# Optimization experiments

Hardware: AMD Instinct MI355X
Metric: run time of the kernel (lower is better)

The kernel has to match this reference:

```python
import jax, jax.numpy as jnp
import numpy as np

B, N, X, Y, W1, W2, D = 2, 6, 8, 8, 8, 8, 128
H, DH = 4, 32
L = X * Y          # number of windows
QT = N * W1 * W2   # tokens per window
EPS = 1e-5


def _ln(x, g, b):
    m = x.mean(-1, keepdims=True)
    v = ((x - m) ** 2).mean(-1, keepdims=True)
    return (x - m) * jax.lax.rsqrt(v + EPS) * g + b


def _win(t):
    # b n x y w1 w2 d -> b (x y) (n w1 w2) d
    return t.transpose(0, 2, 3, 1, 4, 5, 6).reshape(B, L, QT, D)


def setup_inputs() -> dict:
    key = jax.random.key(0)
    ks = jax.random.split(key, 12)
    s = 0.02
    inp = {
        'q': jax.random.normal(ks[0], (B, N, X, Y, W1, W2, D), jnp.float32),
        'k': jax.random.normal(ks[1], (B, N, X, Y, W1, W2, D), jnp.float32),
        'v': jax.random.normal(ks[2], (B, N, X, Y, W1, W2, D), jnp.float32),
        'skip': jax.random.normal(ks[3], (B, X, Y, W1, W2, D), jnp.float32),
        'gq': jnp.ones((D,), jnp.float32), 'betq': jnp.zeros((D,), jnp.float32),
        'gk': jnp.ones((D,), jnp.float32), 'betk': jnp.zeros((D,), jnp.float32),
        'gv': jnp.ones((D,), jnp.float32), 'betv': jnp.zeros((D,), jnp.float32),
        'wq': jax.random.normal(ks[4], (D, H * DH), jnp.float32) * s,
        'bq': jnp.zeros((H * DH,), jnp.float32),
        'wk': jax.random.normal(ks[5], (D, H * DH), jnp.float32) * s,
        'bk': jnp.zeros((H * DH,), jnp.float32),
        'wv': jax.random.normal(ks[6], (D, H * DH), jnp.float32) * s,
        'bv': jnp.zeros((H * DH,), jnp.float32),
        'wp': jax.random.normal(ks[7], (H * DH, D), jnp.float32) * s,
        'bp': jnp.zeros((D,), jnp.float32),
    }
    return inp


def reference(q, k, v, skip, gq, betq, gk, betk, gv, betv,
              wq, bq, wk, bk, wv, bv, wp, bp):
    scale = DH ** -0.5
    qw, kw, vw = _win(q), _win(k), _win(v)
    # LayerNorm + Linear QKV, split heads: (b, l, T, h, dh)
    qh = (_ln(qw, gq, betq) @ wq + bq).reshape(B, L, QT, H, DH)
    kh = (_ln(kw, gk, betk) @ wk + bk).reshape(B, L, QT, H, DH)
    vh = (_ln(vw, gv, betv) @ wv + bv).reshape(B, L, QT, H, DH)
    dot = scale * jnp.einsum('blqhd,blkhd->bhlqk', qh, kh)
    att = jax.nn.softmax(dot, axis=-1)
    a = jnp.einsum('bhlqk,blkhd->blqhd', att, vh).reshape(B, L, QT, H * DH)
    # b (x y) (n w1 w2) d -> b n x y w1 w2 d
    a = a.reshape(B, X, Y, N, W1, W2, H * DH).transpose(0, 3, 1, 2, 4, 5, 6)
    z = a @ wp + bp
    z = z.mean(1)  # average over views
    return z + skip
```

## Files before the change

### kernel.cpp

```cpp
#include <hip/hip_runtime.h>


typedef unsigned short u16;
typedef __bf16 bf16x8 __attribute__((ext_vector_type(8)));
typedef __bf16 bf16x4 __attribute__((ext_vector_type(4)));
typedef float  f32x16 __attribute__((ext_vector_type(16)));
typedef unsigned short u16x8 __attribute__((ext_vector_type(8)));
typedef unsigned short u16x4 __attribute__((ext_vector_type(4)));

union U8 { u16x8 u; bf16x8 b; u16x4 h[2]; };

#if __has_builtin(__builtin_amdgcn_exp2f)
#define EXP2(x) __builtin_amdgcn_exp2f(x)
#else
#define EXP2(x) exp2f(x)
#endif

__device__ __forceinline__ f32x16 mfma_bf16(bf16x8 a, bf16x8 b, f32x16 c){
  return __builtin_amdgcn_mfma_f32_32x32x16_bf16(a, b, c, 0, 0, 0);
}


__global__ __launch_bounds__(512) void k_prep(
    const float* __restrict__ wq, const float* __restrict__ bq,
    const float* __restrict__ gq, const float* __restrict__ betq,
    const float* __restrict__ wk, const float* __restrict__ bk,
    const float* __restrict__ gk, const float* __restrict__ betk,
    const float* __restrict__ wv, const float* __restrict__ bv,
    const float* __restrict__ gv, const float* __restrict__ betv,
    const float* __restrict__ wp,
    u16* __restrict__ wqT, u16* __restrict__ wkT, u16* __restrict__ wvT, u16* __restrict__ wpT,
    float* __restrict__ bq2, float* __restrict__ bk2, float* __restrict__ bv2,
    float* __restrict__ uq2, float* __restrict__ uk2, float* __restrict__ uv2)
{
  __shared__ float wls[128*33];
  __shared__ float gls[128], bls[128];
  __shared__ float redb[128], redu[128];
  const float ALPHA_Q = 0.17677669529663687f * 1.4426950408889634f;
  int bid = blockIdx.x, tid = threadIdx.x;
  int wsel = bid >> 2, chunk = bid & 3;
  const float *w, *bb, *g, *bet; u16* wT; float *b2, *u2; float alpha;
  if (wsel == 0){ w=wq; bb=bq; g=gq; bet=betq; wT=wqT; b2=bq2; u2=uq2; alpha=ALPHA_Q; }
  else if (wsel == 1){ w=wk; bb=bk; g=gk; bet=betk; wT=wkT; b2=bk2; u2=uk2; alpha=1.f; }
  else if (wsel == 2){ w=wv; bb=bv; g=gv; bet=betv; wT=wvT; b2=bv2; u2=uv2; alpha=1.f; }
  else { w=wp; bb=nullptr; g=nullptr; bet=nullptr; wT=wpT; b2=nullptr; u2=nullptr; alpha=1.f; }

  if (tid < 128){
    gls[tid] = g ? g[tid] : 1.f;
    bls[tid] = bet ? bet[tid] : 0.f;
  }
  const float4* w4 = (const float4*)w;
  #pragma unroll
  for (int i = 0; i < 2; i++){
    int idx = tid + i*512;
    int row = idx >> 3, f4c = idx & 7;
    float4 x = w4[row*32 + chunk*8 + f4c];
    wls[row*33 + f4c*4 + 0] = x.x;
    wls[row*33 + f4c*4 + 1] = x.y;
    wls[row*33 + f4c*4 + 2] = x.z;
    wls[row*33 + f4c*4 + 3] = x.w;
  }
  __syncthreads();
  if (tid < 128){
    int nl = tid >> 2, qp = tid & 3;
    float sb = 0.f, su = 0.f;
    alignas(16) __bf16 tmp[32];
    #pragma unroll
    for (int kk = 0; kk < 32; kk++){
      int k2 = qp*32 + kk;
      float wv_ = wls[k2*33 + nl];
      float gv_ = gls[k2];
      sb += bls[k2] * wv_;
      su += gv_ * wv_;
      tmp[kk] = (__bf16)(wv_ * gv_ * alpha);
    }
    int n = chunk*32 + nl;
    #pragma unroll
    for (int j = 0; j < 4; j++)
      *(bf16x8*)(wT + n*128 + qp*32 + j*8) = *(bf16x8*)&tmp[j*8];
    redb[tid] = sb; redu[tid] = su;
  }
  __syncthreads();
  if (tid < 128){
    int nl = tid >> 2, qp = tid & 3;
    if (qp == 0 && bb){
      int n = chunk*32 + nl;
      float s = bb[n] + redb[tid] + redb[tid+1] + redb[tid+2] + redb[tid+3];
      float u = redu[tid] + redu[tid+1] + redu[tid+2] + redu[tid+3];
      b2[n] = s * alpha;
      u2[n] = u * alpha;
    }
  }
}

__global__ __launch_bounds__(256) void k_lnproj(
    const float* __restrict__ qg, const float* __restrict__ kg, const float* __restrict__ vg,
    const u16* __restrict__ wqT, const u16* __restrict__ wkT, const u16* __restrict__ wvT,
    const float* __restrict__ bq2, const float* __restrict__ bk2, const float* __restrict__ bv2,
    const float* __restrict__ uq2, const float* __restrict__ uk2, const float* __restrict__ uv2,
    u16* __restrict__ qh, u16* __restrict__ kh, u16* __restrict__ vh)
{
  __shared__ alignas(16) u16 Abf[64*136];
  __shared__ float s1s[64], s2s[64];
  int bid = blockIdx.x, tid = threadIdx.x;
  int which = bid % 3;
  int t = bid / 3;
  int n = t % 6, bl = t / 6;
  const float* src; const u16* wT; const float *b2, *u2; u16* dstb;
  if (which == 0){ src=qg; wT=wqT; b2=bq2; u2=uq2; dstb=qh; }
  else if (which == 1){ src=kg; wT=wkT; b2=bk2; u2=uk2; dstb=kh; }
  else { src=vg; wT=wvT; b2=bv2; u2=uv2; dstb=vh; }
  int b = bl >> 6, l = bl & 63;
  const float4* s4 = (const float4*)(src + (size_t)((b*6 + n)*64 + l)*64*128);
  int row = tid >> 2, j = tid & 3;
  float s1 = 0.f, s2 = 0.f;
  #pragma unroll
  for (int i = 0; i < 8; i++){
    float4 xv = s4[row*32 + i*4 + j];
    s1 += xv.x + xv.y + xv.z + xv.w;
    s2 += xv.x*xv.x + xv.y*xv.y + xv.z*xv.z + xv.w*xv.w;
    bf16x4 pk;
    pk[0] = (__bf16)xv.x; pk[1] = (__bf16)xv.y;
    pk[2] = (__bf16)xv.z; pk[3] = (__bf16)xv.w;
    *(bf16x4*)&Abf[row*136 + (i*4 + j)*4] = pk;
  }
  s1 += __shfl_xor(s1, 1, 64); s1 += __shfl_xor(s1, 2, 64);
  s2 += __shfl_xor(s2, 1, 64); s2 += __shfl_xor(s2, 2, 64);
  if (j == 0){
    float m = s1 * (1.f/128.f);
    float r = rsqrtf(s2 * (1.f/128.f) - m*m + 1e-5f);
    s1s[row] = r;
    s2s[row] = r * m;
  }
  __syncthreads();
  int wave = tid >> 6, lane = tid & 63, lm = lane & 31, lh = lane >> 5;
  bf16x8 bfr[8];
  const u16* wrow = wT + (32*wave + lm)*128 + lh*8;
  #pragma unroll
  for (int ks = 0; ks < 8; ks++) bfr[ks] = *(const bf16x8*)(wrow + ks*16);
  f32x16 acc0, acc1;
  #pragma unroll
  for (int r = 0; r < 16; r++){ acc0[r]=0.f; acc1[r]=0.f; }
  #pragma unroll
  for (int ks = 0; ks < 8; ks++){
    bf16x8 a0 = *(const bf16x8*)&Abf[lm*136       + ks*16 + lh*8];
    bf16x8 a1 = *(const bf16x8*)&Abf[(32+lm)*136  + ks*16 + lh*8];
    acc0 = mfma_bf16(a0, bfr[ks], acc0);
    acc1 = mfma_bf16(a1, bfr[ks], acc1);
  }
  int col = 32*wave + lm;
  float u2c = u2[col], bc = b2[col];
  __syncthreads();
  #pragma unroll
  for (int r = 0; r < 16; r++){
    int row0 = (r&3) + 8*(r>>2) + 4*lh;
    float y0 = s1s[row0]     * acc0[r] - s2s[row0]     * u2c + bc;
    float y1 = s1s[row0+32]  * acc1[r] - s2s[row0+32]  * u2c + bc;
    *(__bf16*)&Abf[row0*136 + col]      = (__bf16)y0;
    *(__bf16*)&Abf[(32+row0)*136 + col] = (__bf16)y1;
  }
  __syncthreads();
  #pragma unroll
  for (int i = 0; i < 4; i++){
    int c = tid + i*256;
    int grp = c >> 8, rw = (c >> 2) & 63, part = c & 3;
    u16x8 val = *(const u16x8*)&Abf[rw*136 + grp*32 + part*8];
    *(u16x8*)(dstb + ((size_t)(bl*4 + grp)*384 + n*64 + rw)*32 + part*8) = val;
  }
}

__global__ __launch_bounds__(768, 3) void k_attn(
    const u16* __restrict__ qh, const u16* __restrict__ kh, const u16* __restrict__ vh,
    u16* __restrict__ abar)
{
  extern __shared__ __align__(16) char smem[];
  int bid = blockIdx.x, tid = threadIdx.x;
  int wave = tid >> 6, lane = tid & 63, lm = lane & 31, lh = lane >> 5;
  int grp = (wave >= 6) ? 1 : 0;
  int n = wave - 6*grp;
  int tl = tid - 384*grp;
  int bh = bid + 256*grp;
  int h = bh & 3, bl = bh >> 2;

  u16*   vts    = (u16*)  (smem + grp*25088);
  float* abar_s = (float*)(smem + 50176 + grp*8192);

  const u16* qb = qh + (size_t)bh * 12288;
  const u16* kb = kh + (size_t)bh * 12288;
  const u16* vb = vh + (size_t)bh * 12288;

  const u16* qbase = qb + (size_t)(n*64 + lm)*32 + lh*8;
  bf16x8 qfA0 = *(const bf16x8*)(qbase);
  bf16x8 qfA1 = *(const bf16x8*)(qbase + 16);
  bf16x8 qfB0 = *(const bf16x8*)(qbase + 32*32);
  bf16x8 qfB1 = *(const bf16x8*)(qbase + 32*32 + 16);

  #pragma unroll
  for (int i = 0; i < 4; i++){
    int c = tl + i*384;
    int key = c >> 2, part = c & 3;
    int u = key & 31, tt = key >> 5;
    int a = u >> 2;
    int anew = (a & 4) | ((a & 1) << 1) | ((a >> 1) & 1);
    int pos = tt*32 + anew*4 + (u & 3);
    u16x8 vv = *(const u16x8*)(vb + key*32 + part*8);
    #pragma unroll
    for (int jj = 0; jj < 8; jj++) vts[(part*8 + jj)*392 + pos] = vv[jj];
  }
  for (int idx = tl; idx < 2048; idx += 384) abar_s[idx] = 0.f;
  __syncthreads();

  const u16* vrow = &vts[lm*392 + 8*lh];
  const u16* krow = kb + lm*32 + lh*8;

  f32x16 oA, oB;
  #pragma unroll
  for (int r = 0; r < 16; r++){ oA[r] = 0.f; oB[r] = 0.f; }
  float sleA = 0.f, sleB = 0.f;

  #pragma unroll
  for (int kt = 0; kt < 12; kt++){
    bf16x8 kf0 = *(const bf16x8*)(krow + kt*1024);
    bf16x8 kf1 = *(const bf16x8*)(krow + kt*1024 + 16);
    f32x16 sa, sb_;
    #pragma unroll
    for (int r = 0; r < 16; r++){ sa[r] = 0.f; sb_[r] = 0.f; }
    __builtin_amdgcn_s_setprio(1);
    sa  = mfma_bf16(kf0, qfA0, sa);
    sb_ = mfma_bf16(kf0, qfB0, sb_);
    sa  = mfma_bf16(kf1, qfA1, sa);
    sb_ = mfma_bf16(kf1, qfB1, sb_);
    __builtin_amdgcn_s_setprio(0);
    U8 v0, v1;
    v0.u = *(const u16x8*)(vrow + kt*32);
    v1.u = *(const u16x8*)(vrow + kt*32 + 16);
    U8 pA0, pA1, pB0, pB1;
    #pragma unroll
    for (int r = 0; r < 8; r++){
      float eA0 = EXP2(sa[r]);
      float eA1 = EXP2(sa[r+8]);
      float eB0 = EXP2(sb_[r]);
      float eB1 = EXP2(sb_[r+8]);
      sleA += eA0 + eA1;
      sleB += eB0 + eB1;
      pA0.b[r] = (__bf16)eA0;
      pA1.b[r] = (__bf16)eA1;
      pB0.b[r] = (__bf16)eB0;
      pB1.b[r] = (__bf16)eB1;
    }
    __builtin_amdgcn_s_setprio(1);
    oA = mfma_bf16(pA0.b, v0.b, oA);
    oB = mfma_bf16(pB0.b, v0.b, oB);
    oA = mfma_bf16(pA1.b, v1.b, oA);
    oB = mfma_bf16(pB1.b, v1.b, oB);
    __builtin_amdgcn_s_setprio(0);
  }

  sleA += __shfl_xor(sleA, 32, 64);
  sleB += __shfl_xor(sleB, 32, 64);
  float invA = (1.f/6.f) / sleA;
  float invB = (1.f/6.f) / sleB;

  #pragma unroll
  for (int r = 0; r < 16; r++){
    int q_l = (r&3) + 8*(r>>2) + 4*lh;
    float a = oA[r] * __shfl(invA, q_l, 64);
    float b = oB[r] * __shfl(invB, q_l, 64);
    atomicAdd(&abar_s[q_l*32 + lm], a);
    atomicAdd(&abar_s[(32 + q_l)*32 + lm], b);
  }
  __syncthreads();
  u16* ob = abar + (size_t)(bl*64)*128 + h*32;
  for (int idx = tl; idx < 2048; idx += 384){
    int w12 = idx >> 5, dh = idx & 31;
    *(__bf16*)&ob[(size_t)w12*128 + dh] = (__bf16)abar_s[idx];
  }
}

__global__ __launch_bounds__(256) void k_out(
    const u16* __restrict__ abar, const u16* __restrict__ wpT,
    const float* __restrict__ bp, const float* __restrict__ skip,
    float* __restrict__ out)
{
  __shared__ alignas(16) u16 Als[32*136];
  int tid = threadIdx.x;
  int R0 = blockIdx.x * 32;
  #pragma unroll
  for (int i = 0; i < 2; i++){
    int c = tid + i*256;
    int row = c >> 4, part = c & 15;
    *(u16x8*)&Als[row*136 + part*8] = *(const u16x8*)(abar + (size_t)(R0+row)*128 + part*8);
  }
  __syncthreads();
  int wave = tid >> 6, lane = tid & 63, lm = lane & 31, lh = lane >> 5;
  bf16x8 bfr[8];
  const u16* wrow = wpT + (32*wave + lm)*128 + lh*8;
  #pragma unroll
  for (int ks = 0; ks < 8; ks++) bfr[ks] = *(const bf16x8*)(wrow + ks*16);
  f32x16 acc;
  #pragma unroll
  for (int r = 0; r < 16; r++) acc[r] = 0.f;
  #pragma unroll
  for (int ks = 0; ks < 8; ks++){
    bf16x8 a0 = *(const bf16x8*)&Als[lm*136 + ks*16 + lh*8];
    acc = mfma_bf16(a0, bfr[ks], acc);
  }
  float bias = bp[32*wave + lm];
  #pragma unroll
  for (int r = 0; r < 16; r++){
    int row0 = (r&3) + 8*(r>>2) + 4*lh;
    size_t f0 = (size_t)(R0 + row0)*128 + 32*wave + lm;
    out[f0] = acc[r] + bias + skip[f0];
  }
}

extern "C" void kernel_launch(void* const* d_in, const int* in_sizes, int n_in,
                              void* d_out, int out_size, void* d_ws, size_t ws_size,
                              hipStream_t stream)
{
  const float* q    = (const float*)d_in[0];
  const float* k    = (const float*)d_in[1];
  const float* v    = (const float*)d_in[2];
  const float* skip = (const float*)d_in[3];
  const float* gq   = (const float*)d_in[4];
  const float* betq = (const float*)d_in[5];
  const float* gk   = (const float*)d_in[6];
  const float* betk = (const float*)d_in[7];
  const float* gv   = (const float*)d_in[8];
  const float* betv = (const float*)d_in[9];
  const float* wq   = (const float*)d_in[10];
  const float* bq   = (const float*)d_in[11];
  const float* wk   = (const float*)d_in[12];
  const float* bk   = (const float*)d_in[13];
  const float* wv   = (const float*)d_in[14];
  const float* bv   = (const float*)d_in[15];
  const float* wp   = (const float*)d_in[16];
  const float* bp   = (const float*)d_in[17];
  float* out = (float*)d_out;

  char* ws = (char*)d_ws;
  u16* wqT = (u16*)ws;
  u16* wkT = wqT + 16384;
  u16* wvT = wkT + 16384;
  u16* wpT = wvT + 16384;
  float* bq2 = (float*)(ws + 131072);
  float* bk2 = bq2 + 128;
  float* bv2 = bk2 + 128;
  float* uq2 = bv2 + 128;
  float* uk2 = uq2 + 128;
  float* uv2 = uk2 + 128;
  u16* qh = (u16*)(ws + 134144);
  u16* kh = qh + 6291456;
  u16* vh = kh + 6291456;
  u16* abar = vh + 6291456;

  k_prep  <<<16,   512, 0, stream>>>(wq,bq,gq,betq, wk,bk,gk,betk, wv,bv,gv,betv, wp,
                                     wqT,wkT,wvT,wpT, bq2,bk2,bv2, uq2,uk2,uv2);
  k_lnproj<<<2304, 256, 0, stream>>>(q,k,v, wqT,wkT,wvT, bq2,bk2,bv2, uq2,uk2,uv2, qh,kh,vh);
  k_attn  <<<256,  768, 86016, stream>>>(qh,kh,vh, abar);
  k_out   <<<256,  256, 0, stream>>>(abar, wpT, bp, skip, out);
}
```

Measured before the change: 199.0 us.

## Fuse output projection into attention kernel with per-head atomic accumulation

Removes the separate output-projection kernel and the bf16 abar intermediate. Each attention block now multiplies its head's averaged attention output by its slice of the projection weights and atomically adds the partial result into the fp32 output, which is zeroed with a memset beforehand. Head 0 also adds the bias and skip. The shared-memory accumulator is padded to a stride of 33 to reduce bank conflicts. In exchange the kernel takes on many global float atomics, a memset, and a non-deterministic summation order.

```diff
diff --git a/kernel.cpp b/kernel.cpp
--- a/kernel.cpp
+++ b/kernel.cpp
@@ -171,7 +171,8 @@
 
 __global__ __launch_bounds__(768, 3) void k_attn(
     const u16* __restrict__ qh, const u16* __restrict__ kh, const u16* __restrict__ vh,
-    u16* __restrict__ abar)
+    const u16* __restrict__ wpT, const float* __restrict__ bp,
+    const float* __restrict__ skip, float* __restrict__ out)
 {
   extern __shared__ __align__(16) char smem[];
   int bid = blockIdx.x, tid = threadIdx.x;
@@ -183,7 +184,7 @@
   int h = bh & 3, bl = bh >> 2;
 
   u16*   vts    = (u16*)  (smem + grp*25088);
-  float* abar_s = (float*)(smem + 50176 + grp*8192);
+  float* abar_s = (float*)(smem + 50176 + grp*8448);
 
   const u16* qb = qh + (size_t)bh * 12288;
   const u16* kb = kh + (size_t)bh * 12288;
@@ -207,7 +208,7 @@
     #pragma unroll
     for (int jj = 0; jj < 8; jj++) vts[(part*8 + jj)*392 + pos] = vv[jj];
   }
-  for (int idx = tl; idx < 2048; idx += 384) abar_s[idx] = 0.f;
+  for (int idx = tl; idx < 2112; idx += 384) abar_s[idx] = 0.f;
   __syncthreads();
 
   const u16* vrow = &vts[lm*392 + 8*lh];
@@ -266,51 +267,42 @@
     int q_l = (r&3) + 8*(r>>2) + 4*lh;
     float a = oA[r] * __shfl(invA, q_l, 64);
     float b = oB[r] * __shfl(invB, q_l, 64);
-    atomicAdd(&abar_s[q_l*32 + lm], a);
-    atomicAdd(&abar_s[(32 + q_l)*32 + lm], b);
-  }
-  __syncthreads();
-  u16* ob = abar + (size_t)(bl*64)*128 + h*32;
-  for (int idx = tl; idx < 2048; idx += 384){
-    int w12 = idx >> 5, dh = idx & 31;
-    *(__bf16*)&ob[(size_t)w12*128 + dh] = (__bf16)abar_s[idx];
-  }
-}
-
-__global__ __launch_bounds__(256) void k_out(
-    const u16* __restrict__ abar, const u16* __restrict__ wpT,
-    const float* __restrict__ bp, const float* __restrict__ skip,
-    float* __restrict__ out)
-{
-  __shared__ alignas(16) u16 Als[32*136];
-  int tid = threadIdx.x;
-  int R0 = blockIdx.x * 32;
-  #pragma unroll
-  for (int i = 0; i < 2; i++){
-    int c = tid + i*256;
-    int row = c >> 4, part = c & 15;
-    *(u16x8*)&Als[row*136 + part*8] = *(const u16x8*)(abar + (size_t)(R0+row)*128 + part*8);
-  }
-  __syncthreads();
-  int wave = tid >> 6, lane = tid & 63, lm = lane & 31, lh = lane >> 5;
-  bf16x8 bfr[8];
-  const u16* wrow = wpT + (32*wave + lm)*128 + lh*8;
-  #pragma unroll
-  for (int ks = 0; ks < 8; ks++) bfr[ks] = *(const bf16x8*)(wrow + ks*16);
-  f32x16 acc;
-  #pragma unroll
-  for (int r = 0; r < 16; r++) acc[r] = 0.f;
-  #pragma unroll
-  for (int ks = 0; ks < 8; ks++){
-    bf16x8 a0 = *(const bf16x8*)&Als[lm*136 + ks*16 + lh*8];
-    acc = mfma_bf16(a0, bfr[ks], acc);
-  }
-  float bias = bp[32*wave + lm];
-  #pragma unroll
-  for (int r = 0; r < 16; r++){
-    int row0 = (r&3) + 8*(r>>2) + 4*lh;
-    size_t f0 = (size_t)(R0 + row0)*128 + 32*wave + lm;
-    out[f0] = acc[r] + bias + skip[f0];
+    atomicAdd(&abar_s[q_l*33 + lm], a);
+    atomicAdd(&abar_s[(32 + q_l)*33 + lm], b);
+  }
+  __syncthreads();
+
+  if ((tl >> 6) < 4){
+    int t = tl >> 6;
+    f32x16 ac0, ac1;
+    #pragma unroll
+    for (int r = 0; r < 16; r++){ ac0[r] = 0.f; ac1[r] = 0.f; }
+    #pragma unroll
+    for (int kh2 = 0; kh2 < 2; kh2++){
+      bf16x8 af0, af1;
+      #pragma unroll
+      for (int j2 = 0; j2 < 8; j2++){
+        af0[j2] = (__bf16)abar_s[lm*33      + kh2*16 + lh*8 + j2];
+        af1[j2] = (__bf16)abar_s[(32+lm)*33 + kh2*16 + lh*8 + j2];
+      }
+      bf16x8 bf_ = *(const bf16x8*)(wpT + (size_t)(32*t + lm)*128 + h*32 + kh2*16 + lh*8);
+      ac0 = mfma_bf16(af0, bf_, ac0);
+      ac1 = mfma_bf16(af1, bf_, ac1);
+    }
+    #pragma unroll
+    for (int r = 0; r < 16; r++){
+      int row0 = (r&3) + 8*(r>>2) + 4*lh;
+      int gcol = t*32 + lm;
+      size_t f0 = (size_t)(bl*64 + row0)*128 + gcol;
+      size_t f1 = (size_t)(bl*64 + 32 + row0)*128 + gcol;
+      float v0p = ac0[r], v1p = ac1[r];
+      if (h == 0){
+        v0p += bp[gcol] + skip[f0];
+        v1p += bp[gcol] + skip[f1];
+      }
+      atomicAdd(&out[f0], v0p);
+      atomicAdd(&out[f1], v1p);
+    }
   }
 }
 
@@ -352,11 +344,10 @@
   u16* qh = (u16*)(ws + 134144);
   u16* kh = qh + 6291456;
   u16* vh = kh + 6291456;
-  u16* abar = vh + 6291456;
-
+
+  hipMemsetAsync(out, 0, out_size, stream);
   k_prep  <<<16,   512, 0, stream>>>(wq,bq,gq,betq, wk,bk,gk,betk, wv,bv,gv,betv, wp,
                                      wqT,wkT,wvT,wpT, bq2,bk2,bv2, uq2,uk2,uv2);
   k_lnproj<<<2304, 256, 0, stream>>>(q,k,v, wqT,wkT,wvT, bq2,bk2,bv2, uq2,uk2,uv2, qh,kh,vh);
-  k_attn  <<<256,  768, 86016, stream>>>(qh,kh,vh, abar);
-  k_out   <<<256,  256, 0, stream>>>(abar, wpT, bp, skip, out);
-}
+  k_attn  <<<256,  768, 86016, stream>>>(qh,kh,vh, wpT, bp, skip, out);
+}
```

Result: slower. 210.3 us (+5.7%).
